# Performance work log

Hardware: AMD Instinct MI355X
Metric: run time of the kernel (lower is better)

The kernel has to match this reference:

```python
import jax, jax.numpy as jnp
import numpy as np

NUM_HEADS = 8
NUM_GROUPS = 8
EPS = 1e-5


def setup_inputs() -> dict:
    key = jax.random.key(0)
    k1, k2, k3 = jax.random.split(key, 3)
    B, C, H, W = 16, 512, 32, 32
    x = jax.random.normal(k1, (B, C, H, W), dtype=jnp.float32)
    gn_w = jnp.ones((C,), jnp.float32)
    gn_b = jnp.zeros((C,), jnp.float32)
    # 1x1 convs are plain GEMMs; scale weights like torch default init (~1/sqrt(C))
    qkv_w = jax.random.normal(k2, (3 * C, C), dtype=jnp.float32) * (1.0 / np.sqrt(C))
    qkv_b = jnp.zeros((3 * C,), jnp.float32)
    proj_w = jax.random.normal(k3, (C, C), dtype=jnp.float32) * (1.0 / np.sqrt(C))
    proj_b = jnp.zeros((C,), jnp.float32)
    return {"x": x, "gn_w": gn_w, "gn_b": gn_b, "qkv_w": qkv_w,
            "qkv_b": qkv_b, "proj_w": proj_w, "proj_b": proj_b}


def _group_norm(x, w, b):
    B, C, H, W = x.shape
    xg = x.reshape(B, NUM_GROUPS, -1)  # [B, G, (C/G)*H*W]
    mu = xg.mean(axis=-1, keepdims=True)
    var = xg.var(axis=-1, keepdims=True)
    xn = ((xg - mu) * jax.lax.rsqrt(var + EPS)).reshape(B, C, H, W)
    return xn * w[None, :, None, None] + b[None, :, None, None]


def reference(x, gn_w, gn_b, qkv_w, qkv_b, proj_w, proj_b):
    B, C, H, W = x.shape
    nh = NUM_HEADS
    d = C // nh
    xn = _group_norm(x, gn_w, gn_b)
    # 1x1 conv == channel GEMM
    qkv = jnp.einsum('oc,bchw->bohw', qkv_w, xn) + qkv_b[None, :, None, None]
    qkv = qkv.reshape(B, 3, nh, d, H * W)
    q, k, v = qkv[:, 0], qkv[:, 1], qkv[:, 2]  # [B, nh, d, N]
    scale = d ** (-0.5)
    attn = jax.nn.softmax(jnp.einsum('bhdi,bhdj->bhij', q, k) * scale, axis=-1)
    o = jnp.einsum('bhij,bhdj->bhdi', attn, v).reshape(B, C, H, W)
    # NOTE: source reassigns x, so residual uses attention output, not input
    return o + (jnp.einsum('oc,bchw->bohw', proj_w, o) + proj_b[None, :, None, None])
```

## Files before the change

### kernel.cpp

```cpp
#include <hip/hip_runtime.h>
#include <math.h>

typedef unsigned short u16;
typedef __attribute__((ext_vector_type(8))) short bf8;
typedef __attribute__((ext_vector_type(4))) short s4v;
typedef __attribute__((ext_vector_type(4))) float f4;

#define MFMA(a, b, c) __builtin_amdgcn_mfma_f32_16x16x32_bf16(a, b, c, 0, 0, 0)

#if defined(__has_builtin)
#if __has_builtin(__builtin_amdgcn_exp2f)
#define EXP2(x) __builtin_amdgcn_exp2f(x)
#endif
#endif
#ifndef EXP2
#define EXP2(x) exp2f(x)
#endif

__device__ __forceinline__ u16 f2bf(float f) {
    unsigned u = __float_as_uint(f);
    u += 0x7fffu + ((u >> 16) & 1u);
    return (u16)(u >> 16);
}
__device__ __forceinline__ float bf2f(u16 h) {
    return __uint_as_float(((unsigned)h) << 16);
}
__device__ __forceinline__ void split2(float v, u16& h, u16& l) {
    h = f2bf(v);
    l = f2bf(v - bf2f(h));
}
__device__ __forceinline__ void ldg_lds16(const u16* g, u16* l) {
    __builtin_amdgcn_global_load_lds(
        (const __attribute__((address_space(1))) unsigned int*)g,
        (__attribute__((address_space(3))) unsigned int*)l, 16, 0, 0);
}

__global__ __launch_bounds__(256) void gn_partial_prep(
    const float* __restrict__ x, float2* __restrict__ partial,
    const float* __restrict__ wq, const float* __restrict__ wp,
    u16* __restrict__ qwh, u16* __restrict__ pwh)
{
    const int tid = threadIdx.x;
    if (blockIdx.x >= 1024) {
        const int i = (blockIdx.x - 1024) * 256 + tid;
        if (i < 786432) qwh[i] = f2bf(wq[i]);
        else            pwh[i - 786432] = f2bf(wp[i - 786432]);
        return;
    }
    const int p = blockIdx.x;
    const float4* x4 = (const float4*)x + (size_t)p * 2048;
    float s = 0.f, ss = 0.f;
    for (int i = tid; i < 2048; i += 256) {
        float4 v = x4[i];
        s  += v.x + v.y + v.z + v.w;
        ss += v.x*v.x + v.y*v.y + v.z*v.z + v.w*v.w;
    }
    for (int off = 32; off > 0; off >>= 1) {
        s  += __shfl_down(s, off);
        ss += __shfl_down(ss, off);
    }
    __shared__ float red[8];
    const int wvi = tid >> 6;
    if ((tid & 63) == 0) { red[wvi] = s; red[4 + wvi] = ss; }
    __syncthreads();
    if (tid == 0)
        partial[p] = make_float2(red[0] + red[1] + red[2] + red[3],
                                 red[4] + red[5] + red[6] + red[7]);
}

__global__ __launch_bounds__(256) void gn_apply(
    const float* __restrict__ x, const float* __restrict__ gw,
    const float* __restrict__ gb, const float2* __restrict__ partial,
    u16* __restrict__ xh)
{
    const int blk = blockIdx.x;
    const int bg = blk >> 3, sc = (blk & 7) * 128;
    const int b = bg >> 3, g = bg & 7;
    const size_t base = (size_t)bg * 65536;
    float s = 0.f, ss = 0.f;
    #pragma unroll
    for (int i = 0; i < 8; ++i) {
        float2 pp = partial[bg*8 + i];
        s += pp.x; ss += pp.y;
    }
    const float mu = s * (1.f / 65536.f);
    const float rstd = rsqrtf(ss * (1.f / 65536.f) - mu * mu + 1e-5f);
    const int tid = threadIdx.x;

    __shared__ float tile[64][65];
    for (int s0 = sc; s0 < sc + 128; s0 += 64) {
        for (int idx = tid; idx < 1024; idx += 256) {
            const int c = idx >> 4, s4i = (idx & 15) * 4;
            const float w = gw[g*64 + c], bb = gb[g*64 + c];
            float4 v = *(const float4*)&x[base + (size_t)c*1024 + s0 + s4i];
            tile[s4i + 0][c] = (v.x - mu)*rstd*w + bb;
            tile[s4i + 1][c] = (v.y - mu)*rstd*w + bb;
            tile[s4i + 2][c] = (v.z - mu)*rstd*w + bb;
            tile[s4i + 3][c] = (v.w - mu)*rstd*w + bb;
        }
        __syncthreads();
        for (int idx = tid; idx < 1024; idx += 256) {
            const int srow = idx >> 4, c4 = (idx & 15) * 4;
            s4v hv;
            #pragma unroll
            for (int j = 0; j < 4; ++j)
                hv[j] = (short)f2bf(tile[srow][c4 + j]);
            const size_t o = ((size_t)b*1024 + s0 + srow)*512 + g*64 + c4;
            *(s4v*)&xh[o] = hv;
        }
        __syncthreads();
    }
}

__global__ __launch_bounds__(256, 4) void qkv_mfma(
    const u16* __restrict__ Ah, const u16* __restrict__ Bh,
    const float* __restrict__ bias,
    u16* __restrict__ qh, u16* __restrict__ kh, u16* __restrict__ vh)
{
    __shared__ u16 smem[2*8192];
    const int tid = threadIdx.x;
    const int wv = tid >> 6, ln = tid & 63;
    const int lr = ln & 15, lg = ln >> 4;
    const int m0 = blockIdx.x * 128;
    const int n0 = blockIdx.y * 128;
    const int b  = blockIdx.z;
    const size_t Abase = ((size_t)b*1024 + m0) * 512;
    const size_t Bbase = (size_t)n0 * 512;
    const int wm = (wv >> 1) * 64, wn = (wv & 1) * 64;
    const int srr = ln >> 3, sg = ln & 7;

    f4 acc[4][4] = {};

    for (int k0 = 0; k0 < 512; k0 += 64) {
        __syncthreads();
        #pragma unroll
        for (int it = 0; it < 8; ++it) {
            const int chunk = wv*8 + it;
            const int plane = chunk >> 4;
            const int row = ((chunk & 15) << 3) + srr;
            const u16* srcp = (plane == 0) ? (Ah + Abase) : (Bh + Bbase);
            const u16* gp = srcp + (size_t)row*512 + k0 + ((sg ^ (row & 7)) << 3);
            ldg_lds16(gp, smem + chunk*512);
        }
        __syncthreads();
        #pragma unroll
        for (int f = 0; f < 2; ++f) {
            bf8 av[4], b0[4];
            #pragma unroll
            for (int mf = 0; mf < 4; ++mf) {
                const int row = wm + mf*16 + lr;
                const int ch = (f*4 + lg) ^ (row & 7);
                av[mf] = *(const bf8*)&smem[row*64 + (ch << 3)];
            }
            #pragma unroll
            for (int nf = 0; nf < 4; ++nf) {
                const int row = wn + nf*16 + lr;
                const int ch = (f*4 + lg) ^ (row & 7);
                b0[nf] = *(const bf8*)&smem[8192 + row*64 + (ch << 3)];
            }
            #pragma unroll
            for (int mf = 0; mf < 4; ++mf)
                #pragma unroll
                for (int nf = 0; nf < 4; ++nf)
                    acc[mf][nf] = MFMA(av[mf], b0[nf], acc[mf][nf]);
        }
    }

    #pragma unroll
    for (int nf = 0; nf < 4; ++nf) {
        const int o = n0 + wn + nf*16 + lr;
        const int which = o >> 9;
        const int hd = (o >> 6) & 7;
        const int dd = o & 63;
        const float bs = bias[o];
        const int bh = b*8 + hd;
        #pragma unroll
        for (int mf = 0; mf < 4; ++mf) {
            const int s = m0 + wm + mf*16 + lg*4;
            if (which == 2) {
                s4v hv;
                #pragma unroll
                for (int r = 0; r < 4; ++r)
                    hv[r] = (short)f2bf(acc[mf][nf][r] + bs);
                const size_t a = ((size_t)bh*64 + dd)*1024 + s;
                *(s4v*)&vh[a] = hv;
            } else {
                const float sc = (which == 0) ? 0.18033688011112042f : 1.f;
                u16* dst = (which == 0) ? qh : kh;
                const size_t a = ((size_t)bh*1024 + s)*64 + dd;
                #pragma unroll
                for (int r = 0; r < 4; ++r)
                    dst[a + (size_t)r*64] = f2bf((acc[mf][nf][r] + bs)*sc);
            }
        }
    }
}

__global__ __launch_bounds__(256, 3) void attn_mfma(
    const u16* __restrict__ qh_, const u16* __restrict__ kh_,
    const u16* __restrict__ vh_,
    u16* __restrict__ oh_, u16* __restrict__ ol_)
{
    __shared__ u16 Kt[2][64][64];
    __shared__ u16 Vt[2][64][64];
    __shared__ u16 Pt[4][2][16][72];
    const int tid = threadIdx.x;
    const int wv = tid >> 6, ln = tid & 63;
    const int lr = ln & 15, lg = ln >> 4;
    const int flat = blockIdx.x + (blockIdx.y << 3);
    const int bh = ((flat & 7) << 4) + (flat >> 6);
    const int q0 = ((flat >> 3) & 7) * 128;
    const size_t qkb = (size_t)bh * 65536;
    const int srr = ln >> 3, sg = ln & 7;

    bf8 qf[2][2];
    #pragma unroll
    for (int ii = 0; ii < 2; ++ii)
        #pragma unroll
        for (int f = 0; f < 2; ++f)
            qf[ii][f] = *(const bf8*)&qh_[qkb
                + (size_t)(q0 + wv*32 + ii*16 + lr)*64 + f*32 + lg*8];

    float lpart[2] = {0.f, 0.f};
    f4 oacc[2][4] = {};

    #pragma unroll
    for (int it = 0; it < 4; ++it) {
        const int chunk = wv*4 + it;
        const int row = (chunk & 7)*8 + srr;
        const u16* gp = (chunk < 8)
            ? kh_ + qkb + (size_t)row*64 + ((sg ^ (row & 7)) << 3)
            : vh_ + qkb + (size_t)row*1024 + ((sg ^ (row & 7)) << 3);
        u16* dst = ((chunk < 8) ? &Kt[0][0][0] : &Vt[0][0][0]) + (chunk & 7)*512;
        ldg_lds16(gp, dst);
    }

    for (int t = 0; t < 16; ++t) {
        const int cur = t & 1;
        const int j0 = t * 64;
        const u16* kbuf = &Kt[cur][0][0];
        const u16* vbuf = &Vt[cur][0][0];

        asm volatile("s_waitcnt vmcnt(0)" ::: "memory");
        __syncthreads();

        if (t < 15) {
            #pragma unroll
            for (int it = 0; it < 4; ++it) {
                const int chunk = wv*4 + it;
                const int row = (chunk & 7)*8 + srr;
                const u16* gp = (chunk < 8)
                    ? kh_ + qkb + (size_t)(j0 + 64 + row)*64
                          + ((sg ^ (row & 7)) << 3)
                    : vh_ + qkb + (size_t)row*1024 + j0 + 64
                          + ((sg ^ (row & 7)) << 3);
                u16* dst = ((chunk < 8) ? &Kt[cur^1][0][0] : &Vt[cur^1][0][0])
                           + (chunk & 7)*512;
                ldg_lds16(gp, dst);
            }
        }

        #pragma unroll
        for (int ii = 0; ii < 2; ++ii) {
            f4 sacc[4] = {};
            #pragma unroll
            for (int jf = 0; jf < 4; ++jf)
                #pragma unroll
                for (int f = 0; f < 2; ++f) {
                    const int row = jf*16 + lr;
                    const int ch = (f*4 + lg) ^ (row & 7);
                    const bf8 kv = *(const bf8*)&kbuf[row*64 + (ch << 3)];
                    sacc[jf] = MFMA(kv, qf[ii][f], sacc[jf]);
                }

            float ps = 0.f;
            #pragma unroll
            for (int jf = 0; jf < 4; ++jf) {
                s4v hv;
                #pragma unroll
                for (int r = 0; r < 4; ++r) {
                    const float p = EXP2(sacc[jf][r]);
                    ps += p;
                    hv[r] = (short)(__float_as_uint(p) >> 16);
                }
                *(s4v*)&Pt[wv][ii][lr][(jf*4 + lg)*4] = hv;
            }
            lpart[ii] += ps;

            #pragma unroll
            for (int f = 0; f < 2; ++f) {
                const bf8 pa = *(const bf8*)&Pt[wv][ii][lr][(f*4 + lg)*8];
                #pragma unroll
                for (int nf = 0; nf < 4; ++nf) {
                    const int row = nf*16 + lr;
                    const int ch = (f*4 + lg) ^ (row & 7);
                    const bf8 vv = *(const bf8*)&vbuf[row*64 + (ch << 3)];
                    oacc[ii][nf] = MFMA(pa, vv, oacc[ii][nf]);
                }
            }
        }
    }

    #pragma unroll
    for (int ii = 0; ii < 2; ++ii) {
        lpart[ii] += __shfl_xor(lpart[ii], 16);
        lpart[ii] += __shfl_xor(lpart[ii], 32);
    }

    const int b = bh >> 3, h = bh & 7;
    #pragma unroll
    for (int ii = 0; ii < 2; ++ii) {
        float inv[4];
        #pragma unroll
        for (int r = 0; r < 4; ++r)
            inv[r] = 1.f / __shfl(lpart[ii], lg*4 + r);
        #pragma unroll
        for (int nf = 0; nf < 4; ++nf) {
            const int dd = nf*16 + lr;
            #pragma unroll
            for (int r = 0; r < 4; ++r) {
                const int s = q0 + wv*32 + ii*16 + lg*4 + r;
                const float val = oacc[ii][nf][r] * inv[r];
                const size_t a = ((size_t)b*1024 + s)*512 + h*64 + dd;
                u16 hh, ll; split2(val, hh, ll);
                oh_[a] = hh;
                ol_[a] = ll;
            }
        }
    }
}

__global__ __launch_bounds__(256, 4) void proj_mfma(
    const u16* __restrict__ Ah, const u16* __restrict__ Al,
    const u16* __restrict__ Bh,
    const float* __restrict__ bias, float* __restrict__ out)
{
    __shared__ u16 smem[2*8192];
    const int tid = threadIdx.x;
    const int wv = tid >> 6, ln = tid & 63;
    const int lr = ln & 15, lg = ln >> 4;
    const int m0 = blockIdx.x * 128;
    const int n0 = blockIdx.y * 128;
    const int b  = blockIdx.z;
    const size_t Abase = ((size_t)b*1024 + m0) * 512;
    const size_t Bbase = (size_t)n0 * 512;
    const int wm = (wv >> 1) * 64, wn = (wv & 1) * 64;
    const int srr = ln >> 3, sg = ln & 7;

    f4 acc[4][4] = {};

    for (int k0 = 0; k0 < 512; k0 += 64) {
        __syncthreads();
        #pragma unroll
        for (int it = 0; it < 8; ++it) {
            const int chunk = wv*8 + it;
            const int plane = chunk >> 4;
            const int row = ((chunk & 15) << 3) + srr;
            const u16* srcp = (plane == 0) ? (Ah + Abase) : (Bh + Bbase);
            const u16* gp = srcp + (size_t)row*512 + k0 + ((sg ^ (row & 7)) << 3);
            ldg_lds16(gp, smem + chunk*512);
        }
        __syncthreads();
        #pragma unroll
        for (int f = 0; f < 2; ++f) {
            bf8 av[4], b0[4];
            #pragma unroll
            for (int mf = 0; mf < 4; ++mf) {
                const int row = wm + mf*16 + lr;
                const int ch = (f*4 + lg) ^ (row & 7);
                av[mf] = *(const bf8*)&smem[row*64 + (ch << 3)];
            }
            #pragma unroll
            for (int nf = 0; nf < 4; ++nf) {
                const int row = wn + nf*16 + lr;
                const int ch = (f*4 + lg) ^ (row & 7);
                b0[nf] = *(const bf8*)&smem[8192 + row*64 + (ch << 3)];
            }
            #pragma unroll
            for (int mf = 0; mf < 4; ++mf)
                #pragma unroll
                for (int nf = 0; nf < 4; ++nf)
                    acc[mf][nf] = MFMA(av[mf], b0[nf], acc[mf][nf]);
        }
    }

    #pragma unroll
    for (int nf = 0; nf < 4; ++nf) {
        const int o = n0 + wn + nf*16 + lr;
        const float bs = bias[o];
        #pragma unroll
        for (int mf = 0; mf < 4; ++mf) {
            const int s = m0 + wm + mf*16 + lg*4;
            const size_t ob = ((size_t)b*1024 + s)*512 + o;
            float4 r;
            r.x = acc[mf][nf][0] + bs + bf2f(Ah[ob])         + bf2f(Al[ob]);
            r.y = acc[mf][nf][1] + bs + bf2f(Ah[ob + 512])   + bf2f(Al[ob + 512]);
            r.z = acc[mf][nf][2] + bs + bf2f(Ah[ob + 1024])  + bf2f(Al[ob + 1024]);
            r.w = acc[mf][nf][3] + bs + bf2f(Ah[ob + 1536])  + bf2f(Al[ob + 1536]);
            *(float4*)&out[((size_t)b*512 + o)*1024 + s] = r;
        }
    }
}

extern "C" void kernel_launch(void* const* d_in, const int* in_sizes, int n_in,
                              void* d_out, int out_size, void* d_ws, size_t ws_size,
                              hipStream_t stream) {
    const float* x      = (const float*)d_in[0];
    const float* gn_w   = (const float*)d_in[1];
    const float* gn_b   = (const float*)d_in[2];
    const float* qkv_w  = (const float*)d_in[3];
    const float* qkv_b  = (const float*)d_in[4];
    const float* proj_w = (const float*)d_in[5];
    const float* proj_b = (const float*)d_in[6];
    float* out = (float*)d_out;

    u16* w = (u16*)d_ws;
    const size_t P = 8388608UL;
    u16* xh = w;
    u16* ol = w + P;
    u16* qh = w + 2*P;
    u16* pwh = w + 3*P;
    u16* kh = w + 4*P;
    u16* vh = w + 6*P;
    u16* oh = xh;
    u16* qwh = (u16*)d_out;
    float2* partial = (float2*)(w + 5*P);

    hipLaunchKernelGGL(gn_partial_prep, dim3(5120), dim3(256), 0, stream,
                       x, partial, qkv_w, proj_w, qwh, pwh);
    hipLaunchKernelGGL(gn_apply, dim3(1024), dim3(256), 0, stream,
                       x, gn_w, gn_b, partial, xh);
    hipLaunchKernelGGL(qkv_mfma, dim3(8, 12, 16), dim3(256), 0, stream,
                       xh, qwh, qkv_b, qh, kh, vh);
    hipLaunchKernelGGL(attn_mfma, dim3(8, 128), dim3(256), 0, stream,
                       qh, kh, vh, oh, ol);
    hipLaunchKernelGGL(proj_mfma, dim3(8, 4, 16), dim3(256), 0, stream,
                       oh, ol, pwh, proj_b, out);
}
```

Before: 128.3 us.

## Halve per-block query tile in attention and swizzle P scratch layout

The attention kernel now gives each block 64 query rows instead of 128, one 16-row tile per wave, and launches twice as many blocks (2048 instead of 1024). Occupancy is raised from 3 to 4 blocks per SM via launch bounds. The per-wave P scratch buffer drops its padding and uses an XOR swizzle to avoid LDS bank conflicts. The cost is that each K/V tile is loaded from global memory twice as often relative to compute, which lowers reuse of the staged K/V data.

```diff
diff --git a/kernel.cpp b/kernel.cpp
--- a/kernel.cpp
+++ b/kernel.cpp
@@ -196,33 +196,31 @@
     }
 }
 
-__global__ __launch_bounds__(256, 3) void attn_mfma(
+__global__ __launch_bounds__(256, 4) void attn_mfma(
     const u16* __restrict__ qh_, const u16* __restrict__ kh_,
     const u16* __restrict__ vh_,
     u16* __restrict__ oh_, u16* __restrict__ ol_)
 {
     __shared__ u16 Kt[2][64][64];
     __shared__ u16 Vt[2][64][64];
-    __shared__ u16 Pt[4][2][16][72];
+    __shared__ u16 Pt[4][16][64];
     const int tid = threadIdx.x;
     const int wv = tid >> 6, ln = tid & 63;
     const int lr = ln & 15, lg = ln >> 4;
-    const int flat = blockIdx.x + (blockIdx.y << 3);
-    const int bh = ((flat & 7) << 4) + (flat >> 6);
-    const int q0 = ((flat >> 3) & 7) * 128;
+    const int flat = blockIdx.x + (blockIdx.y << 4);
+    const int bh = ((flat & 7) << 4) + (flat >> 7);
+    const int q0 = ((flat >> 3) & 15) * 64;
     const size_t qkb = (size_t)bh * 65536;
     const int srr = ln >> 3, sg = ln & 7;
 
-    bf8 qf[2][2];
-    #pragma unroll
-    for (int ii = 0; ii < 2; ++ii)
-        #pragma unroll
-        for (int f = 0; f < 2; ++f)
-            qf[ii][f] = *(const bf8*)&qh_[qkb
-                + (size_t)(q0 + wv*32 + ii*16 + lr)*64 + f*32 + lg*8];
-
-    float lpart[2] = {0.f, 0.f};
-    f4 oacc[2][4] = {};
+    bf8 qf[2];
+    #pragma unroll
+    for (int f = 0; f < 2; ++f)
+        qf[f] = *(const bf8*)&qh_[qkb
+            + (size_t)(q0 + wv*16 + lr)*64 + f*32 + lg*8];
+
+    float lpart = 0.f;
+    f4 oacc[4] = {};
 
     #pragma unroll
     for (int it = 0; it < 4; ++it) {
@@ -260,72 +258,66 @@
             }
         }
 
-        #pragma unroll
-        for (int ii = 0; ii < 2; ++ii) {
-            f4 sacc[4] = {};
-            #pragma unroll
-            for (int jf = 0; jf < 4; ++jf)
-                #pragma unroll
-                for (int f = 0; f < 2; ++f) {
-                    const int row = jf*16 + lr;
-                    const int ch = (f*4 + lg) ^ (row & 7);
-                    const bf8 kv = *(const bf8*)&kbuf[row*64 + (ch << 3)];
-                    sacc[jf] = MFMA(kv, qf[ii][f], sacc[jf]);
-                }
-
-            float ps = 0.f;
-            #pragma unroll
-            for (int jf = 0; jf < 4; ++jf) {
-                s4v hv;
-                #pragma unroll
-                for (int r = 0; r < 4; ++r) {
-                    const float p = EXP2(sacc[jf][r]);
-                    ps += p;
-                    hv[r] = (short)(__float_as_uint(p) >> 16);
-                }
-                *(s4v*)&Pt[wv][ii][lr][(jf*4 + lg)*4] = hv;
-            }
-            lpart[ii] += ps;
-
+        f4 sacc[4] = {};
+        #pragma unroll
+        for (int jf = 0; jf < 4; ++jf)
             #pragma unroll
             for (int f = 0; f < 2; ++f) {
-                const bf8 pa = *(const bf8*)&Pt[wv][ii][lr][(f*4 + lg)*8];
-                #pragma unroll
-                for (int nf = 0; nf < 4; ++nf) {
-                    const int row = nf*16 + lr;
-                    const int ch = (f*4 + lg) ^ (row & 7);
-                    const bf8 vv = *(const bf8*)&vbuf[row*64 + (ch << 3)];
-                    oacc[ii][nf] = MFMA(pa, vv, oacc[ii][nf]);
-                }
-            }
-        }
-    }
-
-    #pragma unroll
-    for (int ii = 0; ii < 2; ++ii) {
-        lpart[ii] += __shfl_xor(lpart[ii], 16);
-        lpart[ii] += __shfl_xor(lpart[ii], 32);
-    }
+                const int row = jf*16 + lr;
+                const int ch = (f*4 + lg) ^ (row & 7);
+                const bf8 kv = *(const bf8*)&kbuf[row*64 + (ch << 3)];
+                sacc[jf] = MFMA(kv, qf[f], sacc[jf]);
+            }
+
+        float ps = 0.f;
+        #pragma unroll
+        for (int jf = 0; jf < 4; ++jf) {
+            s4v hv;
+            #pragma unroll
+            for (int r = 0; r < 4; ++r) {
+                const float p = EXP2(sacc[jf][r]);
+                ps += p;
+                hv[r] = (short)(__float_as_uint(p) >> 16);
+            }
+            const int jfl = jf*4 + lg;
+            const int col = (((jfl >> 1) ^ (lr & 7)) << 3) + (jfl & 1)*4;
+            *(s4v*)&Pt[wv][lr][col] = hv;
+        }
+        lpart += ps;
+
+        #pragma unroll
+        for (int f = 0; f < 2; ++f) {
+            const int pc = ((f*4 + lg) ^ (lr & 7)) << 3;
+            const bf8 pa = *(const bf8*)&Pt[wv][lr][pc];
+            #pragma unroll
+            for (int nf = 0; nf < 4; ++nf) {
+                const int row = nf*16 + lr;
+                const int ch = (f*4 + lg) ^ (row & 7);
+                const bf8 vv = *(const bf8*)&vbuf[row*64 + (ch << 3)];
+                oacc[nf] = MFMA(pa, vv, oacc[nf]);
+            }
+        }
+    }
+
+    lpart += __shfl_xor(lpart, 16);
+    lpart += __shfl_xor(lpart, 32);
 
     const int b = bh >> 3, h = bh & 7;
-    #pragma unroll
-    for (int ii = 0; ii < 2; ++ii) {
-        float inv[4];
-        #pragma unroll
-        for (int r = 0; r < 4; ++r)
-            inv[r] = 1.f / __shfl(lpart[ii], lg*4 + r);
-        #pragma unroll
-        for (int nf = 0; nf < 4; ++nf) {
-            const int dd = nf*16 + lr;
-            #pragma unroll
-            for (int r = 0; r < 4; ++r) {
-                const int s = q0 + wv*32 + ii*16 + lg*4 + r;
-                const float val = oacc[ii][nf][r] * inv[r];
-                const size_t a = ((size_t)b*1024 + s)*512 + h*64 + dd;
-                u16 hh, ll; split2(val, hh, ll);
-                oh_[a] = hh;
-                ol_[a] = ll;
-            }
+    float inv[4];
+    #pragma unroll
+    for (int r = 0; r < 4; ++r)
+        inv[r] = 1.f / __shfl(lpart, lg*4 + r);
+    #pragma unroll
+    for (int nf = 0; nf < 4; ++nf) {
+        const int dd = nf*16 + lr;
+        #pragma unroll
+        for (int r = 0; r < 4; ++r) {
+            const int s = q0 + wv*16 + lg*4 + r;
+            const float val = oacc[nf][r] * inv[r];
+            const size_t a = ((size_t)b*1024 + s)*512 + h*64 + dd;
+            u16 hh, ll; split2(val, hh, ll);
+            oh_[a] = hh;
+            ol_[a] = ll;
         }
     }
 }
@@ -432,7 +424,7 @@
                        x, gn_w, gn_b, partial, xh);
     hipLaunchKernelGGL(qkv_mfma, dim3(8, 12, 16), dim3(256), 0, stream,
                        xh, qwh, qkv_b, qh, kh, vh);
-    hipLaunchKernelGGL(attn_mfma, dim3(8, 128), dim3(256), 0, stream,
+    hipLaunchKernelGGL(attn_mfma, dim3(16, 128), dim3(256), 0, stream,
                        qh, kh, vh, oh, ol);
     hipLaunchKernelGGL(proj_mfma, dim3(8, 4, 16), dim3(256), 0, stream,
                        oh, ol, pwh, proj_b, out);
```

Result: slower. 132.8 us (+3.6%).
